# Kernel optimization log

Measured on AMD Instinct MI355X. Metric: run time of the kernel, lower is better.

Reference implementation:

```python
import jax, jax.numpy as jnp
import numpy as np

N_NODES = 100000
N_EDGES = 1600000
IN_FEAT = 128
EMBED = 64
N_LAYERS = 3
N_CENTROID = 100
N_CLASS = 10
EPS = 1e-12


def setup_inputs() -> dict:
    key = jax.random.key(0)
    ks = jax.random.split(key, 8)
    x = jax.random.normal(ks[0], (N_NODES, IN_FEAT), dtype=jnp.float32)
    edge_index = jax.random.randint(ks[1], (2, N_EDGES), 0, N_NODES, dtype=jnp.int64)
    W_embed = jax.random.normal(ks[2], (EMBED, IN_FEAT), dtype=jnp.float32) / np.sqrt(IN_FEAT)
    W_gcn = jax.random.normal(ks[3], (N_LAYERS, EMBED, EMBED), dtype=jnp.float32) / np.sqrt(EMBED)
    b_gcn = jnp.zeros((N_LAYERS, EMBED), dtype=jnp.float32)
    centroids = jax.random.normal(ks[4], (N_CENTROID, EMBED), dtype=jnp.float32)
    W_out = jax.random.normal(ks[5], (N_CLASS, N_CENTROID), dtype=jnp.float32) / np.sqrt(N_CENTROID)
    b_out = jnp.zeros((N_CLASS,), dtype=jnp.float32)
    return {"x": x, "edge_index": edge_index, "W_embed": W_embed, "W_gcn": W_gcn,
            "b_gcn": b_gcn, "centroids": centroids, "W_out": W_out, "b_out": b_out}


def _gcn_norm(edge_index, n, dtype):
    # add self loops, compute symmetric D^{-1/2}(A+I)D^{-1/2} edge weights
    loops = jnp.arange(n, dtype=edge_index.dtype)
    src = jnp.concatenate([edge_index[0], loops])
    dst = jnp.concatenate([edge_index[1], loops])
    deg = jax.ops.segment_sum(jnp.ones_like(dst, dtype=dtype), dst, num_segments=n)
    dinv = jax.lax.rsqrt(jnp.maximum(deg, 1.0))
    norm = dinv[src] * dinv[dst]  # [E+N]
    return src, dst, norm


def reference(x, edge_index, W_embed, W_gcn, b_gcn, centroids, W_out, b_out):
    n = x.shape[0]
    src, dst, norm = _gcn_norm(edge_index, n, x.dtype)
    # Euclidean manifold: log/exp are identity
    h = x @ W_embed.T  # [N, D]
    for l in range(W_gcn.shape[0]):
        hw = h @ W_gcn[l].T                                   # [N, D]
        msg = hw[src] * norm[:, None]                         # gather  [E+N, D]
        h = jax.ops.segment_sum(msg, dst, num_segments=n)     # scatter [N, D]
        h = jax.nn.relu(h + b_gcn[l])
    # centroid distances: ||h_i - c_k|| via expanded quadratic (avoids [N,K,D])
    h2 = jnp.sum(h * h, axis=-1, keepdims=True)               # [N, 1]
    c2 = jnp.sum(centroids * centroids, axis=-1)[None, :]     # [1, K]
    d2 = jnp.maximum(h2 + c2 - 2.0 * (h @ centroids.T), 0.0)  # [N, K]
    dist = jnp.sqrt(d2 + EPS)
    pooled = dist.mean(axis=0)                                # [K] graph pooling
    return pooled @ W_out.T + b_out                           # [num_class]
```

## Files before the change

kernel.cpp:

```cpp
#include <hip/hip_runtime.h>
#include <hip/hip_bf16.h>

typedef unsigned int uint32;
typedef float floatx2 __attribute__((ext_vector_type(2)));
typedef __attribute__((ext_vector_type(8))) short bf16x8;
typedef __attribute__((ext_vector_type(4))) float f32x4;

#define CHUNK 16384


__global__ __launch_bounds__(256) void k_bhist(const int* __restrict__ dst,
                                               int* __restrict__ bcnt,
                                               int E, int NBUCK, int NCH) {
    __shared__ int h[512];
    int c = blockIdx.x, tid = threadIdx.x;
    for (int i = tid; i < NBUCK; i += 256) h[i] = 0;
    __syncthreads();
    int base = c * CHUNK;
#pragma unroll
    for (int k = 0; k < CHUNK / 256; ++k) {
        int e = base + k * 256 + tid;
        if (e < E) atomicAdd(&h[dst[e] >> 8], 1);
    }
    __syncthreads();
    for (int i = tid; i < NBUCK; i += 256) bcnt[(size_t)i * NCH + c] = h[i];
}

__global__ __launch_bounds__(128) void k_bscan1(const int* __restrict__ bcnt,
                                                int* __restrict__ bofs,
                                                int* __restrict__ btot, int NCH) {
    __shared__ int tmp[128];
    int b = blockIdx.x, t = threadIdx.x;
    int v = (t < NCH) ? bcnt[(size_t)b * NCH + t] : 0;
    tmp[t] = v;
    __syncthreads();
    for (int off = 1; off < 128; off <<= 1) {
        int u = (t >= off) ? tmp[t - off] : 0;
        __syncthreads();
        tmp[t] += u;
        __syncthreads();
    }
    if (t < NCH) bofs[(size_t)b * NCH + t] = tmp[t] - v;
    if (t == 127) btot[b] = tmp[127];
}

__global__ __launch_bounds__(512) void k_bscan2(const int* __restrict__ btot,
                                                int* __restrict__ bbase, int nb,
                                                uint32* __restrict__ sent0,
                                                uint32* __restrict__ sent1) {
    __shared__ int tmp[512];
    int t = threadIdx.x;
    if (t < 8) { sent0[t] = 0; sent1[t] = 0; }
    int v = (t < nb) ? btot[t] : 0;
    tmp[t] = v;
    __syncthreads();
    for (int off = 1; off < 512; off <<= 1) {
        int u = (t >= off) ? tmp[t - off] : 0;
        __syncthreads();
        tmp[t] += u;
        __syncthreads();
    }
    if (t < nb) bbase[t] = tmp[t] - v;
    if (t == nb - 1) bbase[nb] = tmp[t];
}

__global__ __launch_bounds__(256) void k_bscatter(const int* __restrict__ ei,
                                                  const int* __restrict__ bbase,
                                                  const int* __restrict__ bofs,
                                                  uint32* __restrict__ ebuf,
                                                  int E, int NBUCK, int NCH) {
    __shared__ int cur[512];
    int c = blockIdx.x, tid = threadIdx.x;
    for (int i = tid; i < NBUCK; i += 256)
        cur[i] = bbase[i] + bofs[(size_t)i * NCH + c];
    __syncthreads();
    int base = c * CHUNK;
#pragma unroll
    for (int k = 0; k < CHUNK / 256; ++k) {
        int e = base + k * 256 + tid;
        if (e < E) {
            int s = ei[e];
            int d = ei[E + e];
            int p = atomicAdd(&cur[d >> 8], 1);
            ebuf[p] = (uint32)s | ((uint32)(d & 255) << 20);
        }
    }
}

__global__ __launch_bounds__(256) void k_bsort(const uint32* __restrict__ ebuf,
                                               const int* __restrict__ bbase,
                                               int* __restrict__ ssrc,
                                               int2* __restrict__ rc,
                                               float* __restrict__ dinv, int N) {
    __shared__ int h[256];
    __shared__ int sc[256];
    __shared__ int cur[256];
    int b = blockIdx.x, tid = threadIdx.x;
    int beg = bbase[b], end = bbase[b + 1];
    h[tid] = 0;
    __syncthreads();
    for (int j = beg + tid; j < end; j += 256)
        atomicAdd(&h[(ebuf[j] >> 20) & 255], 1);
    __syncthreads();
    int v = h[tid];
    sc[tid] = v;
    __syncthreads();
    for (int off = 1; off < 256; off <<= 1) {
        int u = (tid >= off) ? sc[tid - off] : 0;
        __syncthreads();
        sc[tid] += u;
        __syncthreads();
    }
    int rowbase = beg + sc[tid] - v;
    cur[tid] = rowbase;
    int d = b * 256 + tid;
    if (d < N) {
        rc[d] = make_int2(rowbase, v);
        dinv[d] = rsqrtf((float)(v + 1));
    }
    __syncthreads();
    for (int j = beg + tid; j < end; j += 256) {
        uint32 w = ebuf[j];
        int p = atomicAdd(&cur[(w >> 20) & 255], 1);
        ssrc[p] = (int)(w & 0xFFFFFu);
    }
}


__device__ __forceinline__ short f2bf(float f) {
    __hip_bfloat16 b = __float2bfloat16(f);
    return __builtin_bit_cast(short, b);
}

__device__ __forceinline__ float bf2f(short s) {
    uint32 u = ((uint32)(unsigned short)s) << 16;
    return __builtin_bit_cast(float, u);
}

__device__ __forceinline__ bf16x8 pack_bf16x8(float4 v0, float4 v1) {
    bf16x8 r;
    r[0] = f2bf(v0.x); r[1] = f2bf(v0.y); r[2] = f2bf(v0.z); r[3] = f2bf(v0.w);
    r[4] = f2bf(v1.x); r[5] = f2bf(v1.y); r[6] = f2bf(v1.z); r[7] = f2bf(v1.w);
    return r;
}


__global__ __launch_bounds__(256) void k_embed(const float* __restrict__ x,
                                               const float* __restrict__ We,
                                               short* __restrict__ h, int N) {
    int lane = threadIdx.x & 63;
    int w = threadIdx.x >> 6;
    int l15 = lane & 15;
    int lg = lane >> 4;

    bf16x8 B[4][4];
#pragma unroll
    for (int ct = 0; ct < 4; ++ct) {
        const float* wr = We + (size_t)(ct * 16 + l15) * 128 + lg * 8;
#pragma unroll
        for (int ks = 0; ks < 4; ++ks) {
            float4 v0 = *(const float4*)(wr + ks * 32);
            float4 v1 = *(const float4*)(wr + ks * 32 + 4);
            B[ct][ks] = pack_bf16x8(v0, v1);
        }
    }

    int rowbase = blockIdx.x * 256 + w * 64;

    f32x4 acc[4][4];
#pragma unroll
    for (int rt = 0; rt < 4; ++rt)
#pragma unroll
        for (int ct = 0; ct < 4; ++ct)
            acc[rt][ct] = (f32x4){0.f, 0.f, 0.f, 0.f};

#pragma unroll
    for (int ks = 0; ks < 4; ++ks) {
#pragma unroll
        for (int rt = 0; rt < 4; ++rt) {
            int row = rowbase + rt * 16 + l15;
            row = (row < N) ? row : (N - 1);
            const float* xr = x + (size_t)row * 128 + ks * 32 + lg * 8;
            float4 v0 = *(const float4*)xr;
            float4 v1 = *(const float4*)(xr + 4);
            bf16x8 a = pack_bf16x8(v0, v1);
#pragma unroll
            for (int ct = 0; ct < 4; ++ct)
                acc[rt][ct] = __builtin_amdgcn_mfma_f32_16x16x32_bf16(
                    a, B[ct][ks], acc[rt][ct], 0, 0, 0);
        }
    }

#pragma unroll
    for (int rt = 0; rt < 4; ++rt) {
        int row0 = rowbase + rt * 16 + lg * 4;
#pragma unroll
        for (int r = 0; r < 4; ++r) {
            int row = row0 + r;
            if (row < N) {
#pragma unroll
                for (int ct = 0; ct < 4; ++ct)
                    h[(size_t)row * 64 + ct * 16 + l15] = f2bf(acc[rt][ct][r]);
            }
        }
    }
}


__global__ __launch_bounds__(256) void k_gcn(const short* __restrict__ hin,
                                             const float* __restrict__ Wg,
                                             const float* __restrict__ dinv,
                                             uint32* __restrict__ tab0,
                                             uint32* __restrict__ tab1, int N) {
    int lane = threadIdx.x & 63;
    int w = threadIdx.x >> 6;
    int l15 = lane & 15, lg = lane >> 4;

    bf16x8 A[4][2];
#pragma unroll
    for (int rt = 0; rt < 4; ++rt) {
        const float* wr = Wg + (size_t)(rt * 16 + l15) * 64 + lg * 8;
#pragma unroll
        for (int ks = 0; ks < 2; ++ks) {
            float4 v0 = *(const float4*)(wr + ks * 32);
            float4 v1 = *(const float4*)(wr + ks * 32 + 4);
            A[rt][ks] = pack_bf16x8(v0, v1);
        }
    }

    int nodebase = blockIdx.x * 256 + w * 64;

#pragma unroll
    for (int nt = 0; nt < 4; ++nt) {
        int node = nodebase + nt * 16 + l15;
        int nodec = (node < N) ? node : (N - 1);
        const short* hr = hin + ((size_t)nodec << 6) + lg * 8;

        bf16x8 Bf0 = *(const bf16x8*)(hr);
        bf16x8 Bf1 = *(const bf16x8*)(hr + 32);

        f32x4 acc[4];
#pragma unroll
        for (int rt = 0; rt < 4; ++rt) acc[rt] = (f32x4){0.f, 0.f, 0.f, 0.f};
#pragma unroll
        for (int rt = 0; rt < 4; ++rt)
            acc[rt] = __builtin_amdgcn_mfma_f32_16x16x32_bf16(A[rt][0], Bf0, acc[rt], 0, 0, 0);
#pragma unroll
        for (int rt = 0; rt < 4; ++rt)
            acc[rt] = __builtin_amdgcn_mfma_f32_16x16x32_bf16(A[rt][1], Bf1, acc[rt], 0, 0, 0);

        float s = dinv[nodec];
        if (node < N) {
#pragma unroll
            for (int rt = 0; rt < 4; ++rt) {
                int u = 0;
                u = __builtin_amdgcn_cvt_pk_fp8_f32(acc[rt][0] * s, acc[rt][1] * s, u, false);
                u = __builtin_amdgcn_cvt_pk_fp8_f32(acc[rt][2] * s, acc[rt][3] * s, u, true);
                uint32* tp = (rt < 2) ? tab0 : tab1;
                tp[(size_t)node * 8 + (rt & 1) * 4 + lg] = u;
            }
        }
    }
}


__global__ __launch_bounds__(256) void k_agg(const int2* __restrict__ rc,
                                             const int* __restrict__ ssrc,
                                             const float* __restrict__ dinv,
                                             const uint2* __restrict__ tabh,
                                             short* __restrict__ outh,
                                             const float* __restrict__ bias,
                                             int N, int E) {
    int lane = threadIdx.x & 63;
    int wid = threadIdx.x >> 6;
    int q = lane & 3;
    int g = lane >> 2;
    int dbase = (blockIdx.x * 4 + wid) * 16;
    if (dbase >= N) return;

    int2 r = rc[min(dbase + (lane & 15), N - 1)];
    int beg = __shfl(r.x, g);
    int deg = __shfl(r.y, g);
    int dg = dbase + g;
    if (dg >= N) deg = 0;

    floatx2 a01 = {0.f, 0.f}, a23 = {0.f, 0.f}, a45 = {0.f, 0.f}, a67 = {0.f, 0.f};
    auto accum = [&](uint2 v) {
        a01 += __builtin_amdgcn_cvt_pk_f32_fp8((int)v.x, false);
        a23 += __builtin_amdgcn_cvt_pk_f32_fp8((int)v.x, true);
        a45 += __builtin_amdgcn_cvt_pk_f32_fp8((int)v.y, false);
        a67 += __builtin_amdgcn_cvt_pk_f32_fp8((int)v.y, true);
    };

    accum(tabh[(size_t)((dg < N) ? dg : N) * 4 + q]);

    int m = deg;
    m = max(m, __shfl_xor(m, 4));
    m = max(m, __shfl_xor(m, 8));
    m = max(m, __shfl_xor(m, 16));
    m = max(m, __shfl_xor(m, 32));
    int maxd = __builtin_amdgcn_readfirstlane(m);

    int base4 = lane & 60;
    for (int j = 0; j < maxd; j += 16) {
        int i0 = beg + j + q;
        int i1 = i0 + 4;
        int i2 = i0 + 8;
        int i3 = i0 + 12;
        int ev0 = ssrc[i0 < E ? i0 : 0];
        int ev1 = ssrc[i1 < E ? i1 : 0];
        int ev2 = ssrc[i2 < E ? i2 : 0];
        int ev3 = ssrc[i3 < E ? i3 : 0];
        int t0  = __shfl(ev0, base4 | 0);
        int t1  = __shfl(ev0, base4 | 1);
        int t2  = __shfl(ev0, base4 | 2);
        int t3  = __shfl(ev0, base4 | 3);
        int t4  = __shfl(ev1, base4 | 0);
        int t5  = __shfl(ev1, base4 | 1);
        int t6  = __shfl(ev1, base4 | 2);
        int t7  = __shfl(ev1, base4 | 3);
        int t8  = __shfl(ev2, base4 | 0);
        int t9  = __shfl(ev2, base4 | 1);
        int ta  = __shfl(ev2, base4 | 2);
        int tb  = __shfl(ev2, base4 | 3);
        int tc  = __shfl(ev3, base4 | 0);
        int td  = __shfl(ev3, base4 | 1);
        int te  = __shfl(ev3, base4 | 2);
        int tf  = __shfl(ev3, base4 | 3);
        t0 = (j +  0 < deg) ? t0 : N;
        t1 = (j +  1 < deg) ? t1 : N;
        t2 = (j +  2 < deg) ? t2 : N;
        t3 = (j +  3 < deg) ? t3 : N;
        t4 = (j +  4 < deg) ? t4 : N;
        t5 = (j +  5 < deg) ? t5 : N;
        t6 = (j +  6 < deg) ? t6 : N;
        t7 = (j +  7 < deg) ? t7 : N;
        t8 = (j +  8 < deg) ? t8 : N;
        t9 = (j +  9 < deg) ? t9 : N;
        ta = (j + 10 < deg) ? ta : N;
        tb = (j + 11 < deg) ? tb : N;
        tc = (j + 12 < deg) ? tc : N;
        td = (j + 13 < deg) ? td : N;
        te = (j + 14 < deg) ? te : N;
        tf = (j + 15 < deg) ? tf : N;
        uint2 v0 = tabh[(size_t)t0 * 4 + q];
        uint2 v1 = tabh[(size_t)t1 * 4 + q];
        uint2 v2 = tabh[(size_t)t2 * 4 + q];
        uint2 v3 = tabh[(size_t)t3 * 4 + q];
        uint2 v4 = tabh[(size_t)t4 * 4 + q];
        uint2 v5 = tabh[(size_t)t5 * 4 + q];
        uint2 v6 = tabh[(size_t)t6 * 4 + q];
        uint2 v7 = tabh[(size_t)t7 * 4 + q];
        uint2 v8 = tabh[(size_t)t8 * 4 + q];
        uint2 v9 = tabh[(size_t)t9 * 4 + q];
        uint2 va = tabh[(size_t)ta * 4 + q];
        uint2 vb = tabh[(size_t)tb * 4 + q];
        uint2 vc = tabh[(size_t)tc * 4 + q];
        uint2 vd = tabh[(size_t)td * 4 + q];
        uint2 ve = tabh[(size_t)te * 4 + q];
        uint2 vf = tabh[(size_t)tf * 4 + q];
        accum(v0); accum(v1); accum(v2); accum(v3);
        accum(v4); accum(v5); accum(v6); accum(v7);
        accum(v8); accum(v9); accum(va); accum(vb);
        accum(vc); accum(vd); accum(ve); accum(vf);
    }

    if (dg < N) {
        float dd = dinv[dg];
        float4 b0 = *(const float4*)(bias + q * 8);
        float4 b1 = *(const float4*)(bias + q * 8 + 4);
        bf16x8 o;
        o[0] = f2bf(fmaxf(fmaf(dd, a01.x, b0.x), 0.f));
        o[1] = f2bf(fmaxf(fmaf(dd, a01.y, b0.y), 0.f));
        o[2] = f2bf(fmaxf(fmaf(dd, a23.x, b0.z), 0.f));
        o[3] = f2bf(fmaxf(fmaf(dd, a23.y, b0.w), 0.f));
        o[4] = f2bf(fmaxf(fmaf(dd, a45.x, b1.x), 0.f));
        o[5] = f2bf(fmaxf(fmaf(dd, a45.y, b1.y), 0.f));
        o[6] = f2bf(fmaxf(fmaf(dd, a67.x, b1.z), 0.f));
        o[7] = f2bf(fmaxf(fmaf(dd, a67.y, b1.w), 0.f));
        __builtin_nontemporal_store(o, (bf16x8*)(outh + (size_t)dg * 64 + q * 8));
    }
}


__global__ __launch_bounds__(256) void k_cent(const short* __restrict__ hin,
                                              const float* __restrict__ C,
                                              float* __restrict__ partials, int N) {
    __shared__ float pool4[4][112];
    __shared__ float h2_s[128];
    int tid = threadIdx.x;
    int lane = tid & 63, w = tid >> 6;
    int l15 = lane & 15, lg = lane >> 4;

    bf16x8 B[7][2];
    float c2r[7];
#pragma unroll
    for (int ct = 0; ct < 7; ++ct) {
        int col = ct * 16 + l15;
        float c2p = 0.f;
#pragma unroll
        for (int ks = 0; ks < 2; ++ks) {
            float4 v0 = make_float4(0.f, 0.f, 0.f, 0.f);
            float4 v1 = make_float4(0.f, 0.f, 0.f, 0.f);
            if (col < 100) {
                const float* cr = C + (size_t)col * 64 + ks * 32 + lg * 8;
                v0 = *(const float4*)cr;
                v1 = *(const float4*)(cr + 4);
            }
            B[ct][ks] = pack_bf16x8(v0, v1);
            c2p = fmaf(v0.x, v0.x, c2p); c2p = fmaf(v0.y, v0.y, c2p);
            c2p = fmaf(v0.z, v0.z, c2p); c2p = fmaf(v0.w, v0.w, c2p);
            c2p = fmaf(v1.x, v1.x, c2p); c2p = fmaf(v1.y, v1.y, c2p);
            c2p = fmaf(v1.z, v1.z, c2p); c2p = fmaf(v1.w, v1.w, c2p);
        }
        c2p += __shfl_xor(c2p, 16);
        c2p += __shfl_xor(c2p, 32);
        c2r[ct] = c2p;
    }

    int rowbase = blockIdx.x * 128 + w * 32;

    f32x4 acc[2][7];
#pragma unroll
    for (int rt = 0; rt < 2; ++rt)
#pragma unroll
        for (int ct = 0; ct < 7; ++ct)
            acc[rt][ct] = (f32x4){0.f, 0.f, 0.f, 0.f};

#pragma unroll
    for (int rt = 0; rt < 2; ++rt) {
        int row = rowbase + rt * 16 + l15;
        int rowc = (row < N) ? row : (N - 1);
        const short* hr = hin + ((size_t)rowc << 6) + lg * 8;
        bf16x8 a0 = *(const bf16x8*)(hr);
        bf16x8 a1 = *(const bf16x8*)(hr + 32);

        float h2p = 0.f;
#pragma unroll
        for (int j = 0; j < 8; ++j) {
            float v0 = bf2f(a0[j]);
            float v1 = bf2f(a1[j]);
            h2p = fmaf(v0, v0, h2p);
            h2p = fmaf(v1, v1, h2p);
        }
        h2p += __shfl_xor(h2p, 16);
        h2p += __shfl_xor(h2p, 32);
        if (lg == 0) h2_s[w * 32 + rt * 16 + l15] = h2p;

#pragma unroll
        for (int ct = 0; ct < 7; ++ct)
            acc[rt][ct] = __builtin_amdgcn_mfma_f32_16x16x32_bf16(
                a0, B[ct][0], acc[rt][ct], 0, 0, 0);
#pragma unroll
        for (int ct = 0; ct < 7; ++ct)
            acc[rt][ct] = __builtin_amdgcn_mfma_f32_16x16x32_bf16(
                a1, B[ct][1], acc[rt][ct], 0, 0, 0);
    }

    float S[7] = {0.f, 0.f, 0.f, 0.f, 0.f, 0.f, 0.f};
#pragma unroll
    for (int rt = 0; rt < 2; ++rt) {
#pragma unroll
        for (int r = 0; r < 4; ++r) {
            int row = rowbase + rt * 16 + lg * 4 + r;
            float h2v = h2_s[w * 32 + rt * 16 + lg * 4 + r];
            bool rv = row < N;
#pragma unroll
            for (int ct = 0; ct < 7; ++ct) {
                int col = ct * 16 + l15;
                float G = acc[rt][ct][r];
                float d2 = fmaxf(h2v + c2r[ct] - 2.f * G, 0.f);
                float xx = d2 + 1e-12f;
                float dist = xx * __frsqrt_rn(xx);
                S[ct] += (rv && col < 100) ? dist : 0.f;
            }
        }
    }
#pragma unroll
    for (int ct = 0; ct < 7; ++ct) {
        float s = S[ct];
        s += __shfl_xor(s, 16);
        s += __shfl_xor(s, 32);
        if (lg == 0) pool4[w][ct * 16 + l15] = s;
    }
    __syncthreads();
    if (tid < 112) {
        float s = pool4[0][tid] + pool4[1][tid] + pool4[2][tid] + pool4[3][tid];
        partials[(size_t)blockIdx.x * 128 + tid] = s;
    }
}


__global__ __launch_bounds__(1024) void k_out(const float* __restrict__ partials, int nb,
                                              const float* __restrict__ Wout,
                                              const float* __restrict__ bout,
                                              float* __restrict__ out, float invN) {
    __shared__ float ps[8][112];
    int t = threadIdx.x & 127, g = threadIdx.x >> 7;
    if (t < 112) {
        float s0 = 0.f, s1 = 0.f, s2 = 0.f, s3 = 0.f;
        float s4 = 0.f, s5 = 0.f, s6 = 0.f, s7 = 0.f;
        int b = g;
        for (; b + 56 < nb; b += 64) {
            s0 += partials[(size_t)(b     ) * 128 + t];
            s1 += partials[(size_t)(b +  8) * 128 + t];
            s2 += partials[(size_t)(b + 16) * 128 + t];
            s3 += partials[(size_t)(b + 24) * 128 + t];
            s4 += partials[(size_t)(b + 32) * 128 + t];
            s5 += partials[(size_t)(b + 40) * 128 + t];
            s6 += partials[(size_t)(b + 48) * 128 + t];
            s7 += partials[(size_t)(b + 56) * 128 + t];
        }
        for (; b < nb; b += 8) s0 += partials[(size_t)b * 128 + t];
        ps[g][t] = ((s0 + s1) + (s2 + s3)) + ((s4 + s5) + (s6 + s7));
    }
    __syncthreads();
    if (threadIdx.x < 10) {
        int tt = threadIdx.x;
        float s = 0.f;
        for (int k = 0; k < 100; ++k) {
            float p = ps[0][k] + ps[1][k] + ps[2][k] + ps[3][k]
                    + ps[4][k] + ps[5][k] + ps[6][k] + ps[7][k];
            s = fmaf(p, Wout[tt * 100 + k], s);
        }
        out[tt] = s * invN + bout[tt];
    }
}


extern "C" void kernel_launch(void* const* d_in, const int* in_sizes, int n_in,
                              void* d_out, int out_size, void* d_ws, size_t ws_size,
                              hipStream_t stream) {
    const float* x    = (const float*)d_in[0];
    const int*   ei   = (const int*)d_in[1];
    const float* We   = (const float*)d_in[2];
    const float* Wg   = (const float*)d_in[3];
    const float* bg   = (const float*)d_in[4];
    const float* C    = (const float*)d_in[5];
    const float* Wout = (const float*)d_in[6];
    const float* bout = (const float*)d_in[7];
    float*       out  = (float*)d_out;

    const int N = in_sizes[0] / 128;
    const int E = in_sizes[1] / 2;
    const int NBUCK = (N + 255) >> 8;
    const int NCH = (E + CHUNK - 1) / CHUNK;
    const int NBC = (N + 127) / 128;
    const int NBA = (N + 63) / 64;

    char* ws = (char*)d_ws;
    size_t off = 0;
    auto alloc = [&](size_t bytes) { void* p = ws + off; off += (bytes + 511) & ~(size_t)511; return p; };
    float*  dinv   = (float*)alloc((size_t)N * 4);
    int2*   rc     = (int2*) alloc((size_t)N * 8);
    int*    bcnt   = (int*)  alloc((size_t)NBUCK * NCH * 4);
    int*    bofs   = (int*)  alloc((size_t)NBUCK * NCH * 4);
    int*    btot   = (int*)  alloc((size_t)NBUCK * 4);
    int*    bbase  = (int*)  alloc((size_t)(NBUCK + 1) * 4);
    uint32* ebuf   = (uint32*)alloc((size_t)E * 4);
    int*    ssrc   = (int*)  alloc((size_t)(E + 64) * 4);
    short*  hA     = (short*)alloc((size_t)N * 64 * 2);
    uint32* tab0   = (uint32*)alloc((size_t)(N + 1) * 32);
    uint32* tab1   = (uint32*)alloc((size_t)(N + 1) * 32);
    float*  partials = (float*)alloc((size_t)NBC * 128 * 4);

    k_bhist<<<NCH, 256, 0, stream>>>(ei + E, bcnt, E, NBUCK, NCH);
    k_bscan1<<<NBUCK, 128, 0, stream>>>(bcnt, bofs, btot, NCH);
    k_bscan2<<<1, 512, 0, stream>>>(btot, bbase, NBUCK,
                                    tab0 + (size_t)N * 8, tab1 + (size_t)N * 8);
    k_bscatter<<<NCH, 256, 0, stream>>>(ei, bbase, bofs, ebuf, E, NBUCK, NCH);
    k_bsort<<<NBUCK, 256, 0, stream>>>(ebuf, bbase, ssrc, rc, dinv, N);

    k_embed<<<(N + 255) / 256, 256, 0, stream>>>(x, We, hA, N);

    for (int l = 0; l < 3; ++l) {
        k_gcn<<<(N + 255) / 256, 256, 0, stream>>>(hA, Wg + (size_t)l * 64 * 64,
                                                   dinv, tab0, tab1, N);
        k_agg<<<NBA, 256, 0, stream>>>(rc, ssrc, dinv, (const uint2*)tab0,
                                       hA, bg + (size_t)l * 64, N, E);
        k_agg<<<NBA, 256, 0, stream>>>(rc, ssrc, dinv, (const uint2*)tab1,
                                       hA + 32, bg + (size_t)l * 64 + 32, N, E);
    }

    k_cent<<<NBC, 256, 0, stream>>>(hA, C, partials, N);

    k_out<<<1, 1024, 0, stream>>>(partials, NBC, Wout, bout, out, 1.0f / (float)N);
}
```

Measured before the change: 339.0 us.

## Replace two-level bucket sort CSR build with global-atomic counting sort

Replaces the bucketed histogram/scatter/local-sort pipeline that builds the destination-sorted CSR with a simpler counting sort: per-node degree via global atomics, a three-stage prefix scan, then an atomic scatter of sources into per-row cursors. This removes the intermediate packed edge buffer and the second per-bucket sorting pass, but relies on 1.6M global atomics spread across 100K counters (twice) and gives a nondeterministic order within each row, which can hurt gather locality and make floating-point sums vary between runs.

```diff
diff --git a/kernel.cpp b/kernel.cpp
--- a/kernel.cpp
+++ b/kernel.cpp
@@ -6,48 +6,36 @@
 typedef __attribute__((ext_vector_type(8))) short bf16x8;
 typedef __attribute__((ext_vector_type(4))) float f32x4;
 
-#define CHUNK 16384
-
-
-__global__ __launch_bounds__(256) void k_bhist(const int* __restrict__ dst,
-                                               int* __restrict__ bcnt,
-                                               int E, int NBUCK, int NCH) {
-    __shared__ int h[512];
-    int c = blockIdx.x, tid = threadIdx.x;
-    for (int i = tid; i < NBUCK; i += 256) h[i] = 0;
-    __syncthreads();
-    int base = c * CHUNK;
-#pragma unroll
-    for (int k = 0; k < CHUNK / 256; ++k) {
-        int e = base + k * 256 + tid;
-        if (e < E) atomicAdd(&h[dst[e] >> 8], 1);
-    }
-    __syncthreads();
-    for (int i = tid; i < NBUCK; i += 256) bcnt[(size_t)i * NCH + c] = h[i];
-}
-
-__global__ __launch_bounds__(128) void k_bscan1(const int* __restrict__ bcnt,
-                                                int* __restrict__ bofs,
-                                                int* __restrict__ btot, int NCH) {
-    __shared__ int tmp[128];
-    int b = blockIdx.x, t = threadIdx.x;
-    int v = (t < NCH) ? bcnt[(size_t)b * NCH + t] : 0;
+
+__global__ __launch_bounds__(256) void k_deg(const int* __restrict__ dst,
+                                             int* __restrict__ cnt, int E) {
+    int stride = gridDim.x * 256;
+    for (int e = blockIdx.x * 256 + threadIdx.x; e < E; e += stride)
+        atomicAdd(&cnt[dst[e]], 1);
+}
+
+__global__ __launch_bounds__(256) void k_scan1(const int* __restrict__ cnt,
+                                               int* __restrict__ pfx,
+                                               int* __restrict__ btot, int N) {
+    __shared__ int tmp[256];
+    int b = blockIdx.x, t = threadIdx.x, d = b * 256 + t;
+    int v = (d < N) ? cnt[d] : 0;
     tmp[t] = v;
     __syncthreads();
-    for (int off = 1; off < 128; off <<= 1) {
+    for (int off = 1; off < 256; off <<= 1) {
         int u = (t >= off) ? tmp[t - off] : 0;
         __syncthreads();
         tmp[t] += u;
         __syncthreads();
     }
-    if (t < NCH) bofs[(size_t)b * NCH + t] = tmp[t] - v;
-    if (t == 127) btot[b] = tmp[127];
-}
-
-__global__ __launch_bounds__(512) void k_bscan2(const int* __restrict__ btot,
-                                                int* __restrict__ bbase, int nb,
-                                                uint32* __restrict__ sent0,
-                                                uint32* __restrict__ sent1) {
+    if (d < N) pfx[d] = tmp[t] - v;
+    if (t == 255) btot[b] = tmp[255];
+}
+
+__global__ __launch_bounds__(512) void k_scan2(const int* __restrict__ btot,
+                                               int* __restrict__ bbase, int nb,
+                                               uint32* __restrict__ sent0,
+                                               uint32* __restrict__ sent1) {
     __shared__ int tmp[512];
     int t = threadIdx.x;
     if (t < 8) { sent0[t] = 0; sent1[t] = 0; }
@@ -61,68 +49,33 @@
         __syncthreads();
     }
     if (t < nb) bbase[t] = tmp[t] - v;
-    if (t == nb - 1) bbase[nb] = tmp[t];
-}
-
-__global__ __launch_bounds__(256) void k_bscatter(const int* __restrict__ ei,
-                                                  const int* __restrict__ bbase,
-                                                  const int* __restrict__ bofs,
-                                                  uint32* __restrict__ ebuf,
-                                                  int E, int NBUCK, int NCH) {
-    __shared__ int cur[512];
-    int c = blockIdx.x, tid = threadIdx.x;
-    for (int i = tid; i < NBUCK; i += 256)
-        cur[i] = bbase[i] + bofs[(size_t)i * NCH + c];
-    __syncthreads();
-    int base = c * CHUNK;
-#pragma unroll
-    for (int k = 0; k < CHUNK / 256; ++k) {
-        int e = base + k * 256 + tid;
-        if (e < E) {
-            int s = ei[e];
-            int d = ei[E + e];
-            int p = atomicAdd(&cur[d >> 8], 1);
-            ebuf[p] = (uint32)s | ((uint32)(d & 255) << 20);
-        }
-    }
-}
-
-__global__ __launch_bounds__(256) void k_bsort(const uint32* __restrict__ ebuf,
+}
+
+__global__ __launch_bounds__(256) void k_scan3(const int* __restrict__ cnt,
+                                               const int* __restrict__ pfx,
                                                const int* __restrict__ bbase,
-                                               int* __restrict__ ssrc,
                                                int2* __restrict__ rc,
+                                               int* __restrict__ cur,
                                                float* __restrict__ dinv, int N) {
-    __shared__ int h[256];
-    __shared__ int sc[256];
-    __shared__ int cur[256];
-    int b = blockIdx.x, tid = threadIdx.x;
-    int beg = bbase[b], end = bbase[b + 1];
-    h[tid] = 0;
-    __syncthreads();
-    for (int j = beg + tid; j < end; j += 256)
-        atomicAdd(&h[(ebuf[j] >> 20) & 255], 1);
-    __syncthreads();
-    int v = h[tid];
-    sc[tid] = v;
-    __syncthreads();
-    for (int off = 1; off < 256; off <<= 1) {
-        int u = (tid >= off) ? sc[tid - off] : 0;
-        __syncthreads();
-        sc[tid] += u;
-        __syncthreads();
-    }
-    int rowbase = beg + sc[tid] - v;
-    cur[tid] = rowbase;
-    int d = b * 256 + tid;
+    int d = blockIdx.x * 256 + threadIdx.x;
     if (d < N) {
+        int rowbase = bbase[blockIdx.x] + pfx[d];
+        int v = cnt[d];
         rc[d] = make_int2(rowbase, v);
+        cur[d] = rowbase;
         dinv[d] = rsqrtf((float)(v + 1));
     }
-    __syncthreads();
-    for (int j = beg + tid; j < end; j += 256) {
-        uint32 w = ebuf[j];
-        int p = atomicAdd(&cur[(w >> 20) & 255], 1);
-        ssrc[p] = (int)(w & 0xFFFFFu);
+}
+
+__global__ __launch_bounds__(256) void k_scatter(const int* __restrict__ ei,
+                                                 int* __restrict__ cur,
+                                                 int* __restrict__ ssrc, int E) {
+    int stride = gridDim.x * 256;
+    for (int e = blockIdx.x * 256 + threadIdx.x; e < E; e += stride) {
+        int s = ei[e];
+        int d = ei[E + e];
+        int p = atomicAdd(&cur[d], 1);
+        ssrc[p] = s;
     }
 }
 
@@ -543,8 +496,7 @@
 
     const int N = in_sizes[0] / 128;
     const int E = in_sizes[1] / 2;
-    const int NBUCK = (N + 255) >> 8;
-    const int NCH = (E + CHUNK - 1) / CHUNK;
+    const int NBN = (N + 255) / 256;
     const int NBC = (N + 127) / 128;
     const int NBA = (N + 63) / 64;
 
@@ -553,23 +505,24 @@
     auto alloc = [&](size_t bytes) { void* p = ws + off; off += (bytes + 511) & ~(size_t)511; return p; };
     float*  dinv   = (float*)alloc((size_t)N * 4);
     int2*   rc     = (int2*) alloc((size_t)N * 8);
-    int*    bcnt   = (int*)  alloc((size_t)NBUCK * NCH * 4);
-    int*    bofs   = (int*)  alloc((size_t)NBUCK * NCH * 4);
-    int*    btot   = (int*)  alloc((size_t)NBUCK * 4);
-    int*    bbase  = (int*)  alloc((size_t)(NBUCK + 1) * 4);
-    uint32* ebuf   = (uint32*)alloc((size_t)E * 4);
+    int*    cnt    = (int*)  alloc((size_t)N * 4);
+    int*    pfx    = (int*)  alloc((size_t)N * 4);
+    int*    cur    = (int*)  alloc((size_t)N * 4);
+    int*    btot   = (int*)  alloc((size_t)NBN * 4);
+    int*    bbase  = (int*)  alloc((size_t)(NBN + 1) * 4);
     int*    ssrc   = (int*)  alloc((size_t)(E + 64) * 4);
     short*  hA     = (short*)alloc((size_t)N * 64 * 2);
     uint32* tab0   = (uint32*)alloc((size_t)(N + 1) * 32);
     uint32* tab1   = (uint32*)alloc((size_t)(N + 1) * 32);
     float*  partials = (float*)alloc((size_t)NBC * 128 * 4);
 
-    k_bhist<<<NCH, 256, 0, stream>>>(ei + E, bcnt, E, NBUCK, NCH);
-    k_bscan1<<<NBUCK, 128, 0, stream>>>(bcnt, bofs, btot, NCH);
-    k_bscan2<<<1, 512, 0, stream>>>(btot, bbase, NBUCK,
-                                    tab0 + (size_t)N * 8, tab1 + (size_t)N * 8);
-    k_bscatter<<<NCH, 256, 0, stream>>>(ei, bbase, bofs, ebuf, E, NBUCK, NCH);
-    k_bsort<<<NBUCK, 256, 0, stream>>>(ebuf, bbase, ssrc, rc, dinv, N);
+    hipMemsetAsync(cnt, 0, (size_t)N * 4, stream);
+    k_deg<<<2048, 256, 0, stream>>>(ei + E, cnt, E);
+    k_scan1<<<NBN, 256, 0, stream>>>(cnt, pfx, btot, N);
+    k_scan2<<<1, 512, 0, stream>>>(btot, bbase, NBN,
+                                   tab0 + (size_t)N * 8, tab1 + (size_t)N * 8);
+    k_scan3<<<NBN, 256, 0, stream>>>(cnt, pfx, bbase, rc, cur, dinv, N);
+    k_scatter<<<2048, 256, 0, stream>>>(ei, cur, ssrc, E);
 
     k_embed<<<(N + 255) / 256, 256, 0, stream>>>(x, We, hA, N);
 
```

New measurement: 478.8 us. 41.2% more time.
